# Kernel optimization log

Hardware: AMD Instinct MI355X
Metric: run time of the kernel (lower is better)

Reference implementation:

```python
import math
import jax, jax.numpy as jnp
import numpy as np

N_HEAD = 12

def setup_inputs() -> dict:
    key = jax.random.key(0)
    ks = jax.random.split(key, 5)
    B, T, C = 4, 2048, 768
    s = 0.02
    return {
        "x": jax.random.normal(ks[0], (B, T, C), jnp.float32),
        "W_attn": jax.random.normal(ks[1], (3 * C, C), jnp.float32) * s,
        "b_attn": jax.random.normal(ks[2], (3 * C,), jnp.float32) * s,
        "W_proj": jax.random.normal(ks[3], (C, C), jnp.float32) * s,
        "b_proj": jax.random.normal(ks[4], (C,), jnp.float32) * s,
    }

def reference(x, W_attn, b_attn, W_proj, b_proj):
    B, T, C = x.shape
    H = N_HEAD
    hd = C // H
    qkv = x @ W_attn.T + b_attn                      # [B,T,3C]
    q, k, v = jnp.split(qkv, 3, axis=-1)
    # [B,H,T,hd]
    q = q.reshape(B, T, H, hd).transpose(0, 2, 1, 3)
    k = k.reshape(B, T, H, hd).transpose(0, 2, 1, 3)
    v = v.reshape(B, T, H, hd).transpose(0, 2, 1, 3)
    att = jnp.einsum('bhqd,bhkd->bhqk', q, k) * (1.0 / math.sqrt(hd))
    causal = jnp.tril(jnp.ones((T, T), dtype=bool))  # [T,T]
    att = jnp.where(causal[None, None], att, -jnp.inf)
    att = jax.nn.softmax(att, axis=-1)
    y = jnp.einsum('bhqk,bhkd->bhqd', att, v)        # [B,H,T,hd]
    y = y.transpose(0, 2, 1, 3).reshape(B, T, C)
    return y @ W_proj.T + b_proj
```

## Files before the change

kernel.cpp:

```cpp
#include <hip/hip_runtime.h>
#include <cstdint>

#define T_SEQ 2048
#define C_DIM 768
#define C3    2304
#define NH    12
#define HD    64
#define BT    8192

typedef float f32x4 __attribute__((ext_vector_type(4)));
typedef short s16x8 __attribute__((ext_vector_type(8)));
typedef short s16x4 __attribute__((ext_vector_type(4)));

__device__ __forceinline__ unsigned short bf16_rtne(float x) {
    union { float f; unsigned u; } v; v.f = x;
    unsigned r = (v.u + 0x7FFFu + ((v.u >> 16) & 1u)) >> 16;
    return (unsigned short)r;
}
__device__ __forceinline__ float bf16_tof(unsigned short h) {
    union { float f; unsigned u; } v; v.u = ((unsigned)h) << 16;
    return v.f;
}

__global__ __launch_bounds__(256) void split_bf16(const float* __restrict__ in,
                                                  short* __restrict__ hi,
                                                  short* __restrict__ lo, int n4)
{
    for (int i = blockIdx.x * blockDim.x + threadIdx.x; i < n4; i += gridDim.x * blockDim.x) {
        const float4 v = *(const float4*)&in[(size_t)i * 4];
        unsigned short h0 = bf16_rtne(v.x), h1 = bf16_rtne(v.y),
                       h2 = bf16_rtne(v.z), h3 = bf16_rtne(v.w);
        *(s16x4*)&hi[(size_t)i * 4] = (s16x4){(short)h0, (short)h1, (short)h2, (short)h3};
        *(s16x4*)&lo[(size_t)i * 4] = (s16x4){(short)bf16_rtne(v.x - bf16_tof(h0)),
                                              (short)bf16_rtne(v.y - bf16_tof(h1)),
                                              (short)bf16_rtne(v.z - bf16_tof(h2)),
                                              (short)bf16_rtne(v.w - bf16_tof(h3))};
    }
}

template<int MODE>
__global__ __launch_bounds__(256, 4) void gemm_bt_bf16(
    const short* __restrict__ Ah_g, const short* __restrict__ Al_g,
    const short* __restrict__ Bh_g, const short* __restrict__ Bl_g,
    const float* __restrict__ bias, float* __restrict__ Cout,
    short* __restrict__ Qh, short* __restrict__ Ql,
    short* __restrict__ Kb, short* __restrict__ Vt,
    int M, int N, int K)
{
    __shared__ short Ah[128][40];
    __shared__ short Al[128][40];
    __shared__ short Bh[128][40];
    __shared__ short Bl[128][40];

    const int t    = threadIdx.x;
    const int w    = t >> 6;
    const int lane = t & 63;
    const int lr   = lane & 15;
    const int g    = lane >> 4;
    const int lk   = g * 8;
    const int m0   = blockIdx.y * 128;
    const int n0   = blockIdx.x * 128;
    const int wm   = (w >> 1) * 64;
    const int wn   = (w & 1) * 64;

    f32x4 acc[4][4];
#pragma unroll
    for (int i = 0; i < 4; ++i)
#pragma unroll
        for (int j = 0; j < 4; ++j) acc[i][j] = (f32x4){0.f, 0.f, 0.f, 0.f};

    for (int kk = 0; kk < K; kk += 32) {
#pragma unroll
        for (int i = 0; i < 2; ++i) {
            const int chunk = t + i * 256;
            const int row   = chunk >> 2;
            const int col8  = (chunk & 3) * 8;
            const size_t ga = (size_t)(m0 + row) * K + kk + col8;
            const size_t gb = (size_t)(n0 + row) * K + kk + col8;
            *(s16x8*)&Ah[row][col8] = *(const s16x8*)&Ah_g[ga];
            *(s16x8*)&Al[row][col8] = *(const s16x8*)&Al_g[ga];
            *(s16x8*)&Bh[row][col8] = *(const s16x8*)&Bh_g[gb];
            *(s16x8*)&Bl[row][col8] = *(const s16x8*)&Bl_g[gb];
        }
        __syncthreads();

        s16x8 afh[4], afl[4];
#pragma unroll
        for (int i = 0; i < 4; ++i) {
            afh[i] = *(const s16x8*)&Ah[wm + i * 16 + lr][lk];
            afl[i] = *(const s16x8*)&Al[wm + i * 16 + lr][lk];
        }
#pragma unroll
        for (int j = 0; j < 4; ++j) {
            const s16x8 bfh = *(const s16x8*)&Bh[wn + j * 16 + lr][lk];
            const s16x8 bfl = *(const s16x8*)&Bl[wn + j * 16 + lr][lk];
#pragma unroll
            for (int i = 0; i < 4; ++i) {
                acc[i][j] = __builtin_amdgcn_mfma_f32_16x16x32_bf16(afh[i], bfh, acc[i][j], 0, 0, 0);
                acc[i][j] = __builtin_amdgcn_mfma_f32_16x16x32_bf16(afh[i], bfl, acc[i][j], 0, 0, 0);
                acc[i][j] = __builtin_amdgcn_mfma_f32_16x16x32_bf16(afl[i], bfh, acc[i][j], 0, 0, 0);
            }
        }
        __syncthreads();
    }

    if (MODE == 0) {
#pragma unroll
        for (int j = 0; j < 4; ++j) {
            const float bj = bias[n0 + wn + j * 16 + lr];
#pragma unroll
            for (int i = 0; i < 4; ++i)
#pragma unroll
                for (int r = 0; r < 4; ++r) {
                    const int row = m0 + wm + i * 16 + g * 4 + r;
                    Cout[(size_t)row * N + n0 + wn + j * 16 + lr] = acc[i][j][r] + bj;
                }
        }
    } else {
        const int region = n0 / C_DIM;
#pragma unroll
        for (int j = 0; j < 4; ++j) {
            const int n    = n0 + wn + j * 16 + lr;
            const float bj = bias[n];
            const int nr   = n - region * C_DIM;
            const int hh   = nr >> 6;
            const int d    = nr & 63;
#pragma unroll
            for (int i = 0; i < 4; ++i) {
                const int rowb = m0 + wm + i * 16 + g * 4;
                const int b    = rowb >> 11;
                const int tt   = rowb & 2047;
                const size_t hb = (size_t)b * NH + hh;
                if (region == 0) {
#pragma unroll
                    for (int r = 0; r < 4; ++r) {
                        const float v = (acc[i][j][r] + bj) * 0.125f;
                        const unsigned short hv = bf16_rtne(v);
                        const size_t idx = (hb * T_SEQ + tt + r) * HD + d;
                        Qh[idx] = (short)hv;
                        Ql[idx] = (short)bf16_rtne(v - bf16_tof(hv));
                    }
                } else if (region == 1) {
#pragma unroll
                    for (int r = 0; r < 4; ++r) {
                        const float v = acc[i][j][r] + bj;
                        Kb[(hb * T_SEQ + tt + r) * HD + d] = (short)bf16_rtne(v);
                    }
                } else {
                    s16x4 pv;
#pragma unroll
                    for (int r = 0; r < 4; ++r) pv[r] = (short)bf16_rtne(acc[i][j][r] + bj);
                    *(s16x4*)&Vt[(hb * HD + d) * T_SEQ + tt] = pv;
                }
            }
        }
    }
}

#define NEG_BIG (-3.402823466e+38f)

__global__ __launch_bounds__(512, 8) void flash_attn_bf16(
    const short* __restrict__ Qh, const short* __restrict__ Ql,
    const short* __restrict__ Kb, const short* __restrict__ Vt,
    short* __restrict__ yh, short* __restrict__ yl)
{
    __shared__ short Ks[64][72];
    __shared__ short Vs[64][72];
    __shared__ short Ps[128][72];
    __shared__ float redbuf[128];

    const int t = threadIdx.x;
    const int w = t >> 6;
    const int l = t & 63;
    const int c = l & 15;
    const int g = l >> 4;

    const int qt = gridDim.x - 1 - blockIdx.x;
    const int bh = blockIdx.y;
    const int b  = bh / NH;
    const int hh = bh % NH;
    const int q0 = qt * 128;
    const int qwave = q0 + 16 * w;

    const size_t baseT = (size_t)bh * T_SEQ * HD;
    const size_t baseV = (size_t)bh * HD * T_SEQ;

    s16x8 qfh[2], qfl[2];
#pragma unroll
    for (int ds = 0; ds < 2; ++ds) {
        const size_t qi = baseT + (size_t)(qwave + c) * HD + ds * 32 + g * 8;
        qfh[ds] = *(const s16x8*)&Qh[qi];
        qfl[ds] = *(const s16x8*)&Ql[qi];
    }

    f32x4 o[4];
#pragma unroll
    for (int j = 0; j < 4; ++j) o[j] = (f32x4){0.f, 0.f, 0.f, 0.f};
    float m_run = NEG_BIG, l_run = 0.0f;

    const int nkt = (q0 + 128) / 64;
    for (int kt = 0; kt < nkt; ++kt) {
        const int k0 = kt * 64;
        {
            const int row  = t >> 3;
            const int col8 = (t & 7) * 8;
            *(s16x8*)&Ks[row][col8] = *(const s16x8*)&Kb[baseT + (size_t)(k0 + row) * HD + col8];
            *(s16x8*)&Vs[row][col8] = *(const s16x8*)&Vt[baseV + (size_t)row * T_SEQ + k0 + col8];
        }
        __syncthreads();

        if (k0 <= qwave + 15) {
            f32x4 s[4];
#pragma unroll
            for (int sm = 0; sm < 4; ++sm) {
                s[sm] = (f32x4){0.f, 0.f, 0.f, 0.f};
#pragma unroll
                for (int ds = 0; ds < 2; ++ds) {
                    const s16x8 kf = *(const s16x8*)&Ks[sm * 16 + c][ds * 32 + g * 8];
                    s[sm] = __builtin_amdgcn_mfma_f32_16x16x32_bf16(kf, qfh[ds], s[sm], 0, 0, 0);
                    s[sm] = __builtin_amdgcn_mfma_f32_16x16x32_bf16(kf, qfl[ds], s[sm], 0, 0, 0);
                }
            }

            if (k0 + 63 > qwave) {
                const int qg = qwave + c;
#pragma unroll
                for (int sm = 0; sm < 4; ++sm)
#pragma unroll
                    for (int r = 0; r < 4; ++r)
                        if (k0 + 16 * sm + 4 * g + r > qg) s[sm][r] = NEG_BIG;
            }

            float mt = NEG_BIG;
#pragma unroll
            for (int sm = 0; sm < 4; ++sm)
#pragma unroll
                for (int r = 0; r < 4; ++r) mt = fmaxf(mt, s[sm][r]);
            mt = fmaxf(mt, __shfl_xor(mt, 16));
            mt = fmaxf(mt, __shfl_xor(mt, 32));
            const float mn    = fmaxf(m_run, mt);
            const float alpha = __expf(m_run - mn);
            m_run = mn;

            float ls = 0.0f;
#pragma unroll
            for (int sm = 0; sm < 4; ++sm)
#pragma unroll
                for (int r = 0; r < 4; ++r) {
                    s[sm][r] = __expf(s[sm][r] - mn);
                    ls += s[sm][r];
                }
            ls += __shfl_xor(ls, 16);
            ls += __shfl_xor(ls, 32);
            l_run = l_run * alpha + ls;

            if (g == 0) redbuf[16 * w + c] = alpha;

#pragma unroll
            for (int sm = 0; sm < 4; ++sm)
                *(s16x4*)&Ps[16 * w + c][sm * 16 + g * 4] =
                    (s16x4){(short)bf16_rtne(s[sm][0]), (short)bf16_rtne(s[sm][1]),
                            (short)bf16_rtne(s[sm][2]), (short)bf16_rtne(s[sm][3])};

            {
                float av[4];
#pragma unroll
                for (int r = 0; r < 4; ++r) av[r] = redbuf[16 * w + 4 * g + r];
#pragma unroll
                for (int j = 0; j < 4; ++j)
#pragma unroll
                    for (int r = 0; r < 4; ++r) o[j][r] *= av[r];
            }

#pragma unroll
            for (int ks = 0; ks < 2; ++ks) {
                const s16x8 pf = *(const s16x8*)&Ps[16 * w + c][ks * 32 + g * 8];
#pragma unroll
                for (int j = 0; j < 4; ++j) {
                    const s16x8 vf = *(const s16x8*)&Vs[16 * j + c][ks * 32 + g * 8];
                    o[j] = __builtin_amdgcn_mfma_f32_16x16x32_bf16(pf, vf, o[j], 0, 0, 0);
                }
            }
        }
        __syncthreads();
    }

    if (g == 0) redbuf[16 * w + c] = l_run;
    float linv[4];
#pragma unroll
    for (int r = 0; r < 4; ++r) linv[r] = 1.0f / redbuf[16 * w + 4 * g + r];
#pragma unroll
    for (int j = 0; j < 4; ++j)
#pragma unroll
        for (int r = 0; r < 4; ++r) {
            const float ov = o[j][r] * linv[r];
            const unsigned short hv = bf16_rtne(ov);
            const size_t idx = ((size_t)b * T_SEQ + qwave + 4 * g + r) * C_DIM
                               + hh * HD + 16 * j + c;
            yh[idx] = (short)hv;
            yl[idx] = (short)bf16_rtne(ov - bf16_tof(hv));
        }
}

extern "C" void kernel_launch(void* const* d_in, const int* in_sizes, int n_in,
                              void* d_out, int out_size, void* d_ws, size_t ws_size,
                              hipStream_t stream)
{
    (void)in_sizes; (void)n_in; (void)out_size; (void)ws_size;
    const float* x      = (const float*)d_in[0];
    const float* W_attn = (const float*)d_in[1];
    const float* b_attn = (const float*)d_in[2];
    const float* W_proj = (const float*)d_in[3];
    const float* b_proj = (const float*)d_in[4];
    float* out = (float*)d_out;

    const size_t SX  = (size_t)BT * C_DIM;
    const size_t SWA = (size_t)C3 * C_DIM;
    const size_t SWP = (size_t)C_DIM * C_DIM;

    short* p   = (short*)d_ws;
    short* xh  = p;            p += SX;
    short* xl  = p;            p += SX;
    short* Wah = p;            p += SWA;
    short* Wal = p;            p += SWA;
    short* Wph = p;            p += SWP;
    short* Wpl = p;            p += SWP;
    short* Qh  = p;            p += SX;
    short* Ql  = p;            p += SX;
    short* Kb  = p;            p += SX;
    short* Vt  = p;            p += SX;
    short* yh  = xh;
    short* yl  = xl;

    split_bf16<<<1024, 256, 0, stream>>>(x,      xh,  xl,  (int)(SX  / 4));
    split_bf16<<<512,  256, 0, stream>>>(W_attn, Wah, Wal, (int)(SWA / 4));
    split_bf16<<<256,  256, 0, stream>>>(W_proj, Wph, Wpl, (int)(SWP / 4));

    gemm_bt_bf16<1><<<dim3(C3 / 128, BT / 128), 256, 0, stream>>>(
        xh, xl, Wah, Wal, b_attn, nullptr, Qh, Ql, Kb, Vt, BT, C3, C_DIM);

    flash_attn_bf16<<<dim3(T_SEQ / 128, 4 * NH), 512, 0, stream>>>(Qh, Ql, Kb, Vt, yh, yl);

    gemm_bt_bf16<0><<<dim3(C_DIM / 128, BT / 128), 256, 0, stream>>>(
        yh, yl, Wph, Wpl, b_proj, out, nullptr, nullptr, nullptr, nullptr, BT, C_DIM, C_DIM);
}
```

Baseline: 406.3 us.

## Prefetch next GEMM K-tile into registers and remap blocks per XCD

The GEMM now loads the next K-slice of A/B hi/lo tiles from global memory into registers while the current slice is consumed from LDS, so global latency overlaps the MFMA work. The grid also becomes 1D, with block IDs remapped so that each of the 8 XCDs gets a contiguous range of M rows, which should improve L2 reuse of the A tiles. The prefetch adds register pressure under the 4-blocks-per-CU launch bound and can reduce occupancy or cause spills.

```diff
diff --git a/kernel.cpp b/kernel.cpp
--- a/kernel.cpp
+++ b/kernel.cpp
@@ -38,7 +38,7 @@
     }
 }
 
-template<int MODE>
+template<int MODE, int MBLKS, int NBLKS>
 __global__ __launch_bounds__(256, 4) void gemm_bt_bf16(
     const short* __restrict__ Ah_g, const short* __restrict__ Al_g,
     const short* __restrict__ Bh_g, const short* __restrict__ Bl_g,
@@ -58,31 +58,60 @@
     const int lr   = lane & 15;
     const int g    = lane >> 4;
     const int lk   = g * 8;
-    const int m0   = blockIdx.y * 128;
-    const int n0   = blockIdx.x * 128;
+
+    const int bid = blockIdx.x;
+    const int xcd = bid & 7;
+    const int cix = bid >> 3;
+    const int m0  = (xcd * (MBLKS / 8) + cix / NBLKS) * 128;
+    const int n0  = (cix % NBLKS) * 128;
+
     const int wm   = (w >> 1) * 64;
     const int wn   = (w & 1) * 64;
 
+    const int srow  = t >> 2;
+    const int scol8 = (t & 3) * 8;
+
     f32x4 acc[4][4];
 #pragma unroll
     for (int i = 0; i < 4; ++i)
 #pragma unroll
         for (int j = 0; j < 4; ++j) acc[i][j] = (f32x4){0.f, 0.f, 0.f, 0.f};
 
+    s16x8 pa[2], pal[2], pb[2], pbl[2];
+#pragma unroll
+    for (int i = 0; i < 2; ++i) {
+        const int row   = srow + i * 64;
+        const size_t ga = (size_t)(m0 + row) * K + scol8;
+        const size_t gb = (size_t)(n0 + row) * K + scol8;
+        pa[i]  = *(const s16x8*)&Ah_g[ga];
+        pal[i] = *(const s16x8*)&Al_g[ga];
+        pb[i]  = *(const s16x8*)&Bh_g[gb];
+        pbl[i] = *(const s16x8*)&Bl_g[gb];
+    }
+
     for (int kk = 0; kk < K; kk += 32) {
 #pragma unroll
         for (int i = 0; i < 2; ++i) {
-            const int chunk = t + i * 256;
-            const int row   = chunk >> 2;
-            const int col8  = (chunk & 3) * 8;
-            const size_t ga = (size_t)(m0 + row) * K + kk + col8;
-            const size_t gb = (size_t)(n0 + row) * K + kk + col8;
-            *(s16x8*)&Ah[row][col8] = *(const s16x8*)&Ah_g[ga];
-            *(s16x8*)&Al[row][col8] = *(const s16x8*)&Al_g[ga];
-            *(s16x8*)&Bh[row][col8] = *(const s16x8*)&Bh_g[gb];
-            *(s16x8*)&Bl[row][col8] = *(const s16x8*)&Bl_g[gb];
+            const int row = srow + i * 64;
+            *(s16x8*)&Ah[row][scol8] = pa[i];
+            *(s16x8*)&Al[row][scol8] = pal[i];
+            *(s16x8*)&Bh[row][scol8] = pb[i];
+            *(s16x8*)&Bl[row][scol8] = pbl[i];
         }
         __syncthreads();
+
+        if (kk + 32 < K) {
+#pragma unroll
+            for (int i = 0; i < 2; ++i) {
+                const int row   = srow + i * 64;
+                const size_t ga = (size_t)(m0 + row) * K + kk + 32 + scol8;
+                const size_t gb = (size_t)(n0 + row) * K + kk + 32 + scol8;
+                pa[i]  = *(const s16x8*)&Ah_g[ga];
+                pal[i] = *(const s16x8*)&Al_g[ga];
+                pb[i]  = *(const s16x8*)&Bh_g[gb];
+                pbl[i] = *(const s16x8*)&Bl_g[gb];
+            }
+        }
 
         s16x8 afh[4], afl[4];
 #pragma unroll
@@ -336,11 +365,11 @@
     split_bf16<<<512,  256, 0, stream>>>(W_attn, Wah, Wal, (int)(SWA / 4));
     split_bf16<<<256,  256, 0, stream>>>(W_proj, Wph, Wpl, (int)(SWP / 4));
 
-    gemm_bt_bf16<1><<<dim3(C3 / 128, BT / 128), 256, 0, stream>>>(
+    gemm_bt_bf16<1, 64, 18><<<dim3(64 * 18), 256, 0, stream>>>(
         xh, xl, Wah, Wal, b_attn, nullptr, Qh, Ql, Kb, Vt, BT, C3, C_DIM);
 
     flash_attn_bf16<<<dim3(T_SEQ / 128, 4 * NH), 512, 0, stream>>>(Qh, Ql, Kb, Vt, yh, yl);
 
-    gemm_bt_bf16<0><<<dim3(C_DIM / 128, BT / 128), 256, 0, stream>>>(
+    gemm_bt_bf16<0, 64, 6><<<dim3(64 * 6), 256, 0, stream>>>(
         yh, yl, Wph, Wpl, b_proj, out, nullptr, nullptr, nullptr, nullptr, BT, C_DIM, C_DIM);
 }
```

Measured after the change: 852.6 us. 110% more time.
